# Kernel tuning notes

Measured on AMD Instinct MI355X. Metric: run time of the kernel, lower is better.

The kernel has to match this reference:

```python
import jax, jax.numpy as jnp
import numpy as np

DIM, HEADS, RANK = 768, 12, 64
HEAD_DIM = DIM // HEADS

def _xavier(key, shape):
    fan_in, fan_out = shape[1], shape[0]
    std = (2.0 / (fan_in + fan_out)) ** 0.5
    return std * jax.random.normal(key, shape, dtype=jnp.float32)

def setup_inputs() -> dict:
    key = jax.random.key(0)
    ks = jax.random.split(key, 12)
    B, N = 8, 1024
    x = jax.random.normal(ks[0], (B, N, DIM), dtype=jnp.float32)
    params = {}
    for i, nm in enumerate(['Q', 'K', 'V']):
        params[f'W_{nm}0'] = _xavier(ks[1 + 3 * i], (DIM, RANK))
        params[f'W_{nm}1'] = _xavier(ks[2 + 3 * i], (HEADS, RANK))
        params[f'W_{nm}2'] = _xavier(ks[3 + 3 * i], (HEAD_DIM, RANK))
    proj_w = _xavier(ks[10], (DIM, DIM))
    proj_b = jnp.zeros((DIM,), dtype=jnp.float32)
    return dict(x=x, W_Q0=params['W_Q0'], W_Q1=params['W_Q1'], W_Q2=params['W_Q2'],
                W_K0=params['W_K0'], W_K1=params['W_K1'], W_K2=params['W_K2'],
                W_V0=params['W_V0'], W_V1=params['W_V1'], W_V2=params['W_V2'],
                proj_w=proj_w, proj_b=proj_b)

def _cp_proj(xh, W2, W1, W0, B, N, H, hd):
    # xh: [B,N,H,hd]; contract head_dim with W2 and heads with W1 -> [B,N,R], then expand to dim via W0
    t = jnp.einsum('blnd,dr,nr->blr', xh, W2, W1)
    out = jnp.einsum('blr,mr->blm', t, W0)          # [B,N,dim]
    return out.reshape(B, N, H, hd).transpose(0, 2, 1, 3)  # [B,H,N,hd]

def reference(x, W_Q0, W_Q1, W_Q2, W_K0, W_K1, W_K2, W_V0, W_V1, W_V2, proj_w, proj_b):
    B, N, C = x.shape
    H = W_Q1.shape[0]
    hd = C // H
    scale = hd ** -0.5
    xh = x.reshape(B, N, H, hd)
    q = _cp_proj(xh, W_Q2, W_Q1, W_Q0, B, N, H, hd)
    k = _cp_proj(xh, W_K2, W_K1, W_K0, B, N, H, hd)
    v = _cp_proj(xh, W_V2, W_V1, W_V0, B, N, H, hd)
    attn = jax.nn.softmax(jnp.einsum('bhqd,bhkd->bhqk', q, k) * scale, axis=-1)
    out = jnp.einsum('bhqk,bhkd->bhqd', attn, v).transpose(0, 2, 1, 3).reshape(B, N, C)
    return out @ proj_w.T + proj_b
```

## Files before the change

### kernel.cpp

```cpp
#include <hip/hip_runtime.h>

typedef unsigned short u16;
typedef __attribute__((ext_vector_type(8))) short bf16x8;
typedef __attribute__((ext_vector_type(4))) float f32x4;
typedef __attribute__((ext_vector_type(4))) unsigned short u16x4;
typedef __attribute__((ext_vector_type(8))) unsigned short u16x8;

#define AS1 __attribute__((address_space(1)))
#define AS3 __attribute__((address_space(3)))

__device__ __forceinline__ float b2f(u16 s) {
    return __uint_as_float(((unsigned)s) << 16);
}
__device__ __forceinline__ u16 f2b(float f) {
    unsigned u = __float_as_uint(f);
    unsigned r = 0x7fffu + ((u >> 16) & 1u);
    return (u16)((u + r) >> 16);
}

__device__ __forceinline__ unsigned packtrunc(float p0, float p1) {
#if __has_builtin(__builtin_amdgcn_perm)
    return __builtin_amdgcn_perm(__float_as_uint(p1), __float_as_uint(p0), 0x07060302u);
#else
    return (__float_as_uint(p0) >> 16) | (__float_as_uint(p1) & 0xffff0000u);
#endif
}

__device__ __forceinline__ float truncbf(float p) {
    return __uint_as_float(__float_as_uint(p) & 0xffff0000u);
}

__device__ __forceinline__ void g2l16(const u16* g, u16* l) {
    __builtin_amdgcn_global_load_lds((const AS1 void*)g, (AS3 void*)l, 16, 0, 0);
}

#if __has_builtin(__builtin_amdgcn_exp2f)
#define EXP2(x) __builtin_amdgcn_exp2f(x)
#else
#define EXP2(x) exp2f(x)
#endif

__global__ __launch_bounds__(256) void build_prep(
    const float* __restrict__ Wq0, const float* __restrict__ Wq1, const float* __restrict__ Wq2,
    const float* __restrict__ Wk0, const float* __restrict__ Wk1, const float* __restrict__ Wk2,
    const float* __restrict__ Wv0, const float* __restrict__ Wv1, const float* __restrict__ Wv2,
    const float* __restrict__ PW,
    u16* __restrict__ G, u16* __restrict__ MqkT, u16* __restrict__ Dcat)
{
    const int bx = blockIdx.x;
    const int t = threadIdx.x;
    if (bx < 576) {
        const int idx = bx * 256 + t;
        const int row = idx / 768, c = idx - row * 768;
        const int which = row >> 6, r = row & 63;
        const int h = c >> 6, d = c & 63;
        const float* W1 = (which == 0) ? Wq1 : (which == 1) ? Wk1 : Wv1;
        const float* W2 = (which == 0) ? Wq2 : (which == 1) ? Wk2 : Wv2;
        G[idx] = f2b(W1[h * 64 + r] * W2[d * 64 + r]);
    } else if (bx < 624) {
        __shared__ float wq[64 * 65];
        __shared__ float wk[64 * 65];
        const int hq = bx - 576;
        const int h = hq >> 2, quarter = hq & 3;
        const float qs = 0.125f * 1.4426950408889634f;
        for (int i = t; i < 4096; i += 256) {
            const int dd = i >> 6, r = i & 63;
            wq[dd * 65 + r] = Wq0[(h * 64 + dd) * 64 + r] * qs;
            wk[dd * 65 + r] = Wk0[(h * 64 + dd) * 64 + r];
        }
        __syncthreads();
        const int j0 = quarter * 1024 + t * 4;
        const int r2 = j0 >> 6, r1b = j0 & 63;
        u16x4 pk;
#pragma unroll
        for (int jj = 0; jj < 4; ++jj) {
            float acc = 0.f;
#pragma unroll
            for (int dd = 0; dd < 64; ++dd)
                acc += wk[dd * 65 + r2] * wq[dd * 65 + r1b + jj];
            ((u16*)&pk)[jj] = f2b(acc);
        }
        *(u16x4*)(MqkT + (size_t)(h * 64 + r2) * 64 + r1b) = pk;
    } else {
        __shared__ float w0s[64 * 65];
        __shared__ float pws[32 * 65];
        const int hb = bx - 624;
        const int h = hb / 24, mBase = (hb - h * 24) * 32;
        for (int i = t; i < 4096; i += 256) {
            const int d = i >> 6, r = i & 63;
            w0s[d * 65 + r] = Wv0[(h * 64 + d) * 64 + r];
        }
        for (int i = t; i < 2048; i += 256) {
            const int mi = i >> 6, d = i & 63;
            pws[mi * 65 + d] = PW[(size_t)(mBase + mi) * 768 + h * 64 + d];
        }
        __syncthreads();
        const int r = t & 63, mi0 = t >> 6;
        float w0c[64];
#pragma unroll
        for (int d = 0; d < 64; ++d) w0c[d] = w0s[d * 65 + r];
        for (int mi = mi0; mi < 32; mi += 4) {
            float acc = 0.f;
#pragma unroll
            for (int d = 0; d < 64; ++d) acc += pws[mi * 65 + d] * w0c[d];
            Dcat[(size_t)(mBase + mi) * 768 + h * 64 + r] = f2b(acc);
        }
    }
}

__global__ __launch_bounds__(256, 2) void gemm_t(
    const float* __restrict__ X, const u16* __restrict__ G,
    u16* __restrict__ T, u16* __restrict__ tvt)
{
    __shared__ u16 As[64 * 32];
    __shared__ u16 Bs[64 * 32];

    const int tid = threadIdx.x;
    const int lane = tid & 63, wv = tid >> 6;
    const int l15 = lane & 15, quad = lane >> 4;

    const int lin = blockIdx.x + 3 * blockIdx.y;
    const int xcd = lin & 7, j = lin >> 3;
    const int col = j % 3, rowhi = j / 3;
    const int rowBase = (rowhi * 8 + xcd) * 64;
    const int colBase = col * 64;

    const int srow = tid >> 2;
    const int scol = (tid & 3) * 8;
    const float* aS = X + (size_t)(rowBase + srow) * 768 + scol;
    const u16*  bS  = G + (size_t)(colBase + srow) * 768 + scol;

    float4 a0 = *(const float4*)(aS);
    float4 a1 = *(const float4*)(aS + 4);
    int4   b0 = *(const int4*)(bS);

    const f32x4 zero4 = {0.f, 0.f, 0.f, 0.f};
    f32x4 acc[4];
#pragma unroll
    for (int tn = 0; tn < 4; ++tn) acc[tn] = zero4;

    for (int kk = 0; kk < 768; kk += 32) {
        __syncthreads();
        u16x8 ap;
        ap[0] = f2b(a0.x); ap[1] = f2b(a0.y); ap[2] = f2b(a0.z); ap[3] = f2b(a0.w);
        ap[4] = f2b(a1.x); ap[5] = f2b(a1.y); ap[6] = f2b(a1.z); ap[7] = f2b(a1.w);
        *(u16x8*)&As[srow * 32 + scol] = ap;
        *(int4*)&Bs[srow * 32 + scol]  = b0;
        __syncthreads();

        if (kk < 736) {
            a0 = *(const float4*)(aS + kk + 32);
            a1 = *(const float4*)(aS + kk + 36);
            b0 = *(const int4*)(bS + kk + 32);
        }

        const bf16x8 af = *(const bf16x8*)(As + (wv * 16 + l15) * 32 + quad * 8);
#pragma unroll
        for (int tn = 0; tn < 4; ++tn) {
            const bf16x8 bf = *(const bf16x8*)(Bs + (tn * 16 + l15) * 32 + quad * 8);
            acc[tn] = __builtin_amdgcn_mfma_f32_16x16x32_bf16(af, bf, acc[tn], 0, 0, 0);
        }
    }

    if (colBase < 128) {
#pragma unroll
        for (int tn = 0; tn < 4; ++tn) {
            const int c = colBase + tn * 16 + l15;
#pragma unroll
            for (int r = 0; r < 4; ++r) {
                const int grow = rowBase + wv * 16 + quad * 4 + r;
                T[(size_t)grow * 128 + c] = f2b(acc[tn][r]);
            }
        }
    } else {
#pragma unroll
        for (int tn = 0; tn < 4; ++tn) {
            const int rr = tn * 16 + l15;
            const int grow = rowBase + wv * 16 + quad * 4;
            u16x4 pk;
            pk.x = f2b(acc[tn][0]); pk.y = f2b(acc[tn][1]);
            pk.z = f2b(acc[tn][2]); pk.w = f2b(acc[tn][3]);
            *(u16x4*)(tvt + (size_t)rr * 8192 + grow) = pk;
        }
    }
}

__global__ __launch_bounds__(256, 3) void flash_attn9(
    const u16* __restrict__ T, const u16* __restrict__ MqkT,
    const u16* __restrict__ tvt, u16* __restrict__ Z)
{
    const int bh = blockIdx.x;
    const int qt = blockIdx.y;
    const int b = bh / 12, h = bh - b * 12;
    const u16* qp = T + ((size_t)b * 1024 + qt * 128) * 128;
    const u16* kp = T + (size_t)b * 1024 * 128 + 64;
    const u16* vp = tvt + b * 1024;

    __shared__ u16 B0raw[2 * 64 * 72];
    __shared__ u16 B1raw[2 * 64 * 72];

    const int t = threadIdx.x;
    const int lane = t & 63, wv = t >> 6;
    const int l15 = lane & 15, quad = lane >> 4;

    bf16x8 qf[2][2];
#pragma unroll
    for (int qg = 0; qg < 2; ++qg) {
        const u16* qrow = qp + (size_t)(wv * 32 + qg * 16 + l15) * 128;
        qf[qg][0] = *(const bf16x8*)(qrow + quad * 8);
        qf[qg][1] = *(const bf16x8*)(qrow + 32 + quad * 8);
    }

    const int srow = t >> 2;
    const int scol = (t & 3) * 16;
    const int p5 = srow & 31;
    const int lrow = (srow & 32) | ((p5 & 4) << 2) | ((p5 & 16) >> 1)
                   | ((p5 & 8) >> 1) | (p5 & 3);

    int4 kr0 = *(const int4*)(kp + (size_t)srow * 128 + scol);
    int4 kr1 = *(const int4*)(kp + (size_t)srow * 128 + scol + 8);
    int4 vr0 = *(const int4*)(vp + (size_t)srow * 8192 + scol);
    int4 vr1 = *(const int4*)(vp + (size_t)srow * 8192 + scol + 8);

    const f32x4 zero4 = {0.f, 0.f, 0.f, 0.f};
    {
        f32x4 Wt[2][4];
#pragma unroll
        for (int qg = 0; qg < 2; ++qg)
#pragma unroll
            for (int tn = 0; tn < 4; ++tn) Wt[qg][tn] = zero4;
#pragma unroll
        for (int ks = 0; ks < 2; ++ks) {
#pragma unroll
            for (int tn = 0; tn < 4; ++tn) {
                const bf16x8 mb = *(const bf16x8*)(
                    MqkT + (size_t)(h * 64 + tn * 16 + l15) * 64 + ks * 32 + quad * 8);
                Wt[0][tn] = __builtin_amdgcn_mfma_f32_16x16x32_bf16(qf[0][ks], mb, Wt[0][tn], 0, 0, 0);
                Wt[1][tn] = __builtin_amdgcn_mfma_f32_16x16x32_bf16(qf[1][ks], mb, Wt[1][tn], 0, 0, 0);
            }
        }
#pragma unroll
        for (int qg = 0; qg < 2; ++qg)
#pragma unroll
            for (int tn = 0; tn < 4; ++tn)
#pragma unroll
                for (int r = 0; r < 4; ++r)
                    B1raw[(wv * 32 + qg * 16 + quad * 4 + r) * 72 + tn * 16 + l15] =
                        f2b(Wt[qg][tn][r]);
    }
    __syncthreads();
    bf16x8 wf[2][2];
#pragma unroll
    for (int qg = 0; qg < 2; ++qg) {
        wf[qg][0] = *(const bf16x8*)&B1raw[(wv * 32 + qg * 16 + l15) * 72 + quad * 8];
        wf[qg][1] = *(const bf16x8*)&B1raw[(wv * 32 + qg * 16 + l15) * 72 + 32 + quad * 8];
    }

    *(int4*)&B0raw[lrow * 72 + scol]                 = kr0;
    *(int4*)&B0raw[lrow * 72 + scol + 8]             = kr1;
    *(int4*)&B0raw[64 * 72 + srow * 72 + scol]       = vr0;
    *(int4*)&B0raw[64 * 72 + srow * 72 + scol + 8]   = vr1;
    kr0 = *(const int4*)(kp + (size_t)(64 + srow) * 128 + scol);
    kr1 = *(const int4*)(kp + (size_t)(64 + srow) * 128 + scol + 8);
    vr0 = *(const int4*)(vp + (size_t)srow * 8192 + 64 + scol);
    vr1 = *(const int4*)(vp + (size_t)srow * 8192 + 64 + scol + 8);
    __syncthreads();

    f32x4 o_acc[2][4];
    float Lsum[2] = {0.f, 0.f};
#pragma unroll
    for (int qg = 0; qg < 2; ++qg)
#pragma unroll
        for (int tn = 0; tn < 4; ++tn) o_acc[qg][tn] = zero4;

    for (int kt = 0; kt < 16; ++kt) {
        u16* const kb = (kt & 1) ? B1raw : B0raw;
        u16* const vb = kb + 64 * 72;
        if (kt < 15) {
            u16* const kn = (kt & 1) ? B0raw : B1raw;
            *(int4*)&kn[lrow * 72 + scol]               = kr0;
            *(int4*)&kn[lrow * 72 + scol + 8]           = kr1;
            *(int4*)&kn[64 * 72 + srow * 72 + scol]     = vr0;
            *(int4*)&kn[64 * 72 + srow * 72 + scol + 8] = vr1;
            if (kt < 14) {
                kr0 = *(const int4*)(kp + (size_t)((kt + 2) * 64 + srow) * 128 + scol);
                kr1 = *(const int4*)(kp + (size_t)((kt + 2) * 64 + srow) * 128 + scol + 8);
                vr0 = *(const int4*)(vp + (size_t)srow * 8192 + (kt + 2) * 64 + scol);
                vr1 = *(const int4*)(vp + (size_t)srow * 8192 + (kt + 2) * 64 + scol + 8);
            }
        }

        f32x4 Sacc[2][4];
#pragma unroll
        for (int qg = 0; qg < 2; ++qg)
#pragma unroll
            for (int tk = 0; tk < 4; ++tk) Sacc[qg][tk] = zero4;
        __builtin_amdgcn_s_setprio(1);
#pragma unroll
        for (int ks = 0; ks < 2; ++ks) {
#pragma unroll
            for (int tk = 0; tk < 4; ++tk) {
                const bf16x8 kf = *(const bf16x8*)&kb[(tk * 16 + l15) * 72 + ks * 32 + quad * 8];
                Sacc[0][tk] = __builtin_amdgcn_mfma_f32_16x16x32_bf16(kf, wf[0][ks], Sacc[0][tk], 0, 0, 0);
                Sacc[1][tk] = __builtin_amdgcn_mfma_f32_16x16x32_bf16(kf, wf[1][ks], Sacc[1][tk], 0, 0, 0);
            }
        }
        __builtin_amdgcn_s_setprio(0);

        union { bf16x8 v; unsigned u[4]; } pf[2][2];
#pragma unroll
        for (int qg = 0; qg < 2; ++qg)
#pragma unroll
            for (int tk = 0; tk < 4; ++tk) {
                const float p0 = EXP2(Sacc[qg][tk][0]);
                const float p1 = EXP2(Sacc[qg][tk][1]);
                const float p2 = EXP2(Sacc[qg][tk][2]);
                const float p3 = EXP2(Sacc[qg][tk][3]);
                const int g = tk >> 1, hf = (tk & 1) * 2;
                pf[qg][g].u[hf + 0] = packtrunc(p0, p1);
                pf[qg][g].u[hf + 1] = packtrunc(p2, p3);
                Lsum[qg] += (truncbf(p0) + truncbf(p1)) + (truncbf(p2) + truncbf(p3));
            }

        __builtin_amdgcn_s_setprio(1);
#pragma unroll
        for (int g = 0; g < 2; ++g) {
#pragma unroll
            for (int tn = 0; tn < 4; ++tn) {
                const bf16x8 vf = *(const bf16x8*)&vb[(tn * 16 + l15) * 72 + g * 32 + quad * 8];
                o_acc[0][tn] = __builtin_amdgcn_mfma_f32_16x16x32_bf16(pf[0][g].v, vf, o_acc[0][tn], 0, 0, 0);
                o_acc[1][tn] = __builtin_amdgcn_mfma_f32_16x16x32_bf16(pf[1][g].v, vf, o_acc[1][tn], 0, 0, 0);
            }
        }
        __builtin_amdgcn_s_setprio(0);

        __syncthreads();
    }

#pragma unroll
    for (int qg = 0; qg < 2; ++qg) {
        float Ls = Lsum[qg];
        Ls += __shfl_xor(Ls, 16, 64);
        Ls += __shfl_xor(Ls, 32, 64);
#pragma unroll
        for (int r = 0; r < 4; ++r) {
            const float Lv = __shfl(Ls, quad * 4 + r, 64);
            const float inv = 1.0f / Lv;
            const int token = qt * 128 + wv * 32 + qg * 16 + quad * 4 + r;
#pragma unroll
            for (int tn = 0; tn < 4; ++tn) {
                const int col = h * 64 + tn * 16 + l15;
                Z[(size_t)(b * 1024 + token) * 768 + col] = f2b(o_acc[qg][tn][r] * inv);
            }
        }
    }
}

__global__ __launch_bounds__(256, 3) void gemm_out(
    const u16* __restrict__ A, const u16* __restrict__ Bt,
    float* __restrict__ C, const float* __restrict__ bias)
{
    __shared__ u16 As[128 * 32];
    __shared__ u16 Bs[64 * 32];

    const int tid  = threadIdx.x;
    const int lane = tid & 63, wv = tid >> 6;
    const int l15  = lane & 15, quad = lane >> 4;

    const int lin = blockIdx.x + 12 * blockIdx.y;
    const int xcd = lin & 7, j = lin >> 3;
    const int colT = j % 12, rowhi = j / 12;
    const int rowBase = (rowhi * 8 + xcd) * 128;
    const int colBase = colT * 64;

    const int srowA = wv * 32 + (lane >> 2);
    const int srowB = wv * 16 + (lane >> 2);
    const int scol  = (lane & 3) * 8;
    const u16* aSrc = A  + (size_t)(rowBase + srowA) * 768 + scol;
    const u16* bSrc = Bt + (size_t)(colBase + srowB) * 768 + scol;
    u16* aDst = As + wv * 1024;
    u16* bDst = Bs + wv * 512;

    const f32x4 zero4 = {0.f, 0.f, 0.f, 0.f};
    f32x4 acc[2][4];
#pragma unroll
    for (int tm = 0; tm < 2; ++tm)
#pragma unroll
        for (int tn = 0; tn < 4; ++tn) acc[tm][tn] = zero4;

    for (int kk = 0; kk < 768; kk += 32) {
        __syncthreads();
        g2l16(aSrc + kk,            aDst);
        g2l16(aSrc + kk + 16 * 768, aDst + 512);
        g2l16(bSrc + kk,            bDst);
        __syncthreads();

        bf16x8 af[2], bfm[4];
#pragma unroll
        for (int t = 0; t < 2; ++t)
            af[t]  = *(const bf16x8*)(As + (wv * 32 + t * 16 + l15) * 32 + quad * 8);
#pragma unroll
        for (int t = 0; t < 4; ++t)
            bfm[t] = *(const bf16x8*)(Bs + (t * 16 + l15) * 32 + quad * 8);
#pragma unroll
        for (int tm = 0; tm < 2; ++tm)
#pragma unroll
            for (int tn = 0; tn < 4; ++tn)
                acc[tm][tn] = __builtin_amdgcn_mfma_f32_16x16x32_bf16(
                    af[tm], bfm[tn], acc[tm][tn], 0, 0, 0);
    }

#pragma unroll
    for (int tm = 0; tm < 2; ++tm) {
        const int grow = rowBase + wv * 32 + tm * 16 + quad * 4;
#pragma unroll
        for (int tn = 0; tn < 4; ++tn) {
            const int gcol = colBase + tn * 16 + l15;
            const float bv = bias[gcol];
#pragma unroll
            for (int r = 0; r < 4; ++r)
                C[(size_t)(grow + r) * 768 + gcol] = acc[tm][tn][r] + bv;
        }
    }
}

extern "C" void kernel_launch(void* const* d_in, const int* in_sizes, int n_in,
                              void* d_out, int out_size, void* d_ws, size_t ws_size,
                              hipStream_t stream)
{
    const float* x      = (const float*)d_in[0];
    const float* Wq0    = (const float*)d_in[1];
    const float* Wq1    = (const float*)d_in[2];
    const float* Wq2    = (const float*)d_in[3];
    const float* Wk0    = (const float*)d_in[4];
    const float* Wk1    = (const float*)d_in[5];
    const float* Wk2    = (const float*)d_in[6];
    const float* Wv0    = (const float*)d_in[7];
    const float* Wv1    = (const float*)d_in[8];
    const float* Wv2    = (const float*)d_in[9];
    const float* proj_w = (const float*)d_in[10];
    const float* proj_b = (const float*)d_in[11];
    float* outp = (float*)d_out;

    char* ws = (char*)d_ws;
    u16* T    = (u16*)ws;
    u16* tvt  = (u16*)(ws + 2097152);
    u16* G    = (u16*)(ws + 3145728);
    u16* MqkT = (u16*)(ws + 3440640);
    u16* Dcat = (u16*)(ws + 3538944);
    u16* Zcat = (u16*)(ws + 4718592);

    build_prep<<<912, 256, 0, stream>>>(Wq0, Wq1, Wq2, Wk0, Wk1, Wk2, Wv0, Wv1, Wv2,
                                        proj_w, G, MqkT, Dcat);
    gemm_t<<<dim3(3, 128), 256, 0, stream>>>(x, G, T, tvt);
    flash_attn9<<<dim3(96, 8), 256, 0, stream>>>(T, MqkT, tvt, Zcat);
    gemm_out<<<dim3(12, 64), 256, 0, stream>>>(Zcat, Dcat, outp, proj_b);
}
```

Baseline: 178.0 us.

## Compute softmax row sums via MFMA with ones vector and unroll K-loop by two

```diff
diff --git a/kernel.cpp b/kernel.cpp
--- a/kernel.cpp
+++ b/kernel.cpp
@@ -24,10 +24,6 @@
 #else
     return (__float_as_uint(p0) >> 16) | (__float_as_uint(p1) & 0xffff0000u);
 #endif
-}
-
-__device__ __forceinline__ float truncbf(float p) {
-    return __uint_as_float(__float_as_uint(p) & 0xffff0000u);
 }
 
 __device__ __forceinline__ void g2l16(const u16* g, u16* l) {
@@ -185,7 +181,7 @@
     }
 }
 
-__global__ __launch_bounds__(256, 3) void flash_attn9(
+__global__ __launch_bounds__(256, 3) void flash_attn10(
     const u16* __restrict__ T, const u16* __restrict__ MqkT,
     const u16* __restrict__ tvt, u16* __restrict__ Z)
 {
@@ -217,6 +213,12 @@
     const int lrow = (srow & 32) | ((p5 & 4) << 2) | ((p5 & 16) >> 1)
                    | ((p5 & 8) >> 1) | (p5 & 3);
 
+    bf16x8 vone = {};
+    if (l15 == 0) {
+#pragma unroll
+        for (int j = 0; j < 8; ++j) vone[j] = (short)0x3F80;
+    }
+
     int4 kr0 = *(const int4*)(kp + (size_t)srow * 128 + scol);
     int4 kr1 = *(const int4*)(kp + (size_t)srow * 128 + scol + 8);
     int4 vr0 = *(const int4*)(vp + (size_t)srow * 8192 + scol);
@@ -267,84 +269,91 @@
     __syncthreads();
 
     f32x4 o_acc[2][4];
-    float Lsum[2] = {0.f, 0.f};
+    f32x4 Lacc[2] = {zero4, zero4};
 #pragma unroll
     for (int qg = 0; qg < 2; ++qg)
 #pragma unroll
         for (int tn = 0; tn < 4; ++tn) o_acc[qg][tn] = zero4;
 
-    for (int kt = 0; kt < 16; ++kt) {
-        u16* const kb = (kt & 1) ? B1raw : B0raw;
-        u16* const vb = kb + 64 * 72;
-        if (kt < 15) {
-            u16* const kn = (kt & 1) ? B0raw : B1raw;
-            *(int4*)&kn[lrow * 72 + scol]               = kr0;
-            *(int4*)&kn[lrow * 72 + scol + 8]           = kr1;
-            *(int4*)&kn[64 * 72 + srow * 72 + scol]     = vr0;
-            *(int4*)&kn[64 * 72 + srow * 72 + scol + 8] = vr1;
-            if (kt < 14) {
-                kr0 = *(const int4*)(kp + (size_t)((kt + 2) * 64 + srow) * 128 + scol);
-                kr1 = *(const int4*)(kp + (size_t)((kt + 2) * 64 + srow) * 128 + scol + 8);
-                vr0 = *(const int4*)(vp + (size_t)srow * 8192 + (kt + 2) * 64 + scol);
-                vr1 = *(const int4*)(vp + (size_t)srow * 8192 + (kt + 2) * 64 + scol + 8);
-            }
-        }
-
-        f32x4 Sacc[2][4];
-#pragma unroll
-        for (int qg = 0; qg < 2; ++qg)
-#pragma unroll
-            for (int tk = 0; tk < 4; ++tk) Sacc[qg][tk] = zero4;
-        __builtin_amdgcn_s_setprio(1);
-#pragma unroll
-        for (int ks = 0; ks < 2; ++ks) {
-#pragma unroll
-            for (int tk = 0; tk < 4; ++tk) {
-                const bf16x8 kf = *(const bf16x8*)&kb[(tk * 16 + l15) * 72 + ks * 32 + quad * 8];
-                Sacc[0][tk] = __builtin_amdgcn_mfma_f32_16x16x32_bf16(kf, wf[0][ks], Sacc[0][tk], 0, 0, 0);
-                Sacc[1][tk] = __builtin_amdgcn_mfma_f32_16x16x32_bf16(kf, wf[1][ks], Sacc[1][tk], 0, 0, 0);
-            }
-        }
-        __builtin_amdgcn_s_setprio(0);
-
-        union { bf16x8 v; unsigned u[4]; } pf[2][2];
-#pragma unroll
-        for (int qg = 0; qg < 2; ++qg)
-#pragma unroll
-            for (int tk = 0; tk < 4; ++tk) {
-                const float p0 = EXP2(Sacc[qg][tk][0]);
-                const float p1 = EXP2(Sacc[qg][tk][1]);
-                const float p2 = EXP2(Sacc[qg][tk][2]);
-                const float p3 = EXP2(Sacc[qg][tk][3]);
-                const int g = tk >> 1, hf = (tk & 1) * 2;
-                pf[qg][g].u[hf + 0] = packtrunc(p0, p1);
-                pf[qg][g].u[hf + 1] = packtrunc(p2, p3);
-                Lsum[qg] += (truncbf(p0) + truncbf(p1)) + (truncbf(p2) + truncbf(p3));
-            }
-
-        __builtin_amdgcn_s_setprio(1);
-#pragma unroll
-        for (int g = 0; g < 2; ++g) {
-#pragma unroll
-            for (int tn = 0; tn < 4; ++tn) {
-                const bf16x8 vf = *(const bf16x8*)&vb[(tn * 16 + l15) * 72 + g * 32 + quad * 8];
-                o_acc[0][tn] = __builtin_amdgcn_mfma_f32_16x16x32_bf16(pf[0][g].v, vf, o_acc[0][tn], 0, 0, 0);
-                o_acc[1][tn] = __builtin_amdgcn_mfma_f32_16x16x32_bf16(pf[1][g].v, vf, o_acc[1][tn], 0, 0, 0);
-            }
-        }
-        __builtin_amdgcn_s_setprio(0);
-
-        __syncthreads();
-    }
+#define STAGE(NB)                                                               \
+    {                                                                           \
+        *(int4*)&NB[lrow * 72 + scol]               = kr0;                      \
+        *(int4*)&NB[lrow * 72 + scol + 8]           = kr1;                      \
+        *(int4*)&NB[64 * 72 + srow * 72 + scol]     = vr0;                      \
+        *(int4*)&NB[64 * 72 + srow * 72 + scol + 8] = vr1;                      \
+    }
+#define PREFETCH(KT)                                                            \
+    {                                                                           \
+        kr0 = *(const int4*)(kp + (size_t)((KT) * 64 + srow) * 128 + scol);     \
+        kr1 = *(const int4*)(kp + (size_t)((KT) * 64 + srow) * 128 + scol + 8); \
+        vr0 = *(const int4*)(vp + (size_t)srow * 8192 + (KT) * 64 + scol);      \
+        vr1 = *(const int4*)(vp + (size_t)srow * 8192 + (KT) * 64 + scol + 8);  \
+    }
+#define FLASH_TILE(KB)                                                          \
+    {                                                                           \
+        f32x4 Sacc[2][4];                                                       \
+        _Pragma("unroll")                                                       \
+        for (int qg = 0; qg < 2; ++qg)                                          \
+            _Pragma("unroll")                                                   \
+            for (int tk = 0; tk < 4; ++tk) Sacc[qg][tk] = zero4;                \
+        _Pragma("unroll")                                                       \
+        for (int ks = 0; ks < 2; ++ks) {                                        \
+            _Pragma("unroll")                                                   \
+            for (int tk = 0; tk < 4; ++tk) {                                    \
+                const bf16x8 kf = *(const bf16x8*)&KB[(tk * 16 + l15) * 72 + ks * 32 + quad * 8]; \
+                Sacc[0][tk] = __builtin_amdgcn_mfma_f32_16x16x32_bf16(kf, wf[0][ks], Sacc[0][tk], 0, 0, 0); \
+                Sacc[1][tk] = __builtin_amdgcn_mfma_f32_16x16x32_bf16(kf, wf[1][ks], Sacc[1][tk], 0, 0, 0); \
+            }                                                                   \
+        }                                                                       \
+        union { bf16x8 v; unsigned u[4]; } pf[2][2];                            \
+        _Pragma("unroll")                                                       \
+        for (int qg = 0; qg < 2; ++qg)                                          \
+            _Pragma("unroll")                                                   \
+            for (int tk = 0; tk < 4; ++tk) {                                    \
+                const float p0 = EXP2(Sacc[qg][tk][0]);                         \
+                const float p1 = EXP2(Sacc[qg][tk][1]);                         \
+                const float p2 = EXP2(Sacc[qg][tk][2]);                         \
+                const float p3 = EXP2(Sacc[qg][tk][3]);                         \
+                const int g = tk >> 1, hf = (tk & 1) * 2;                       \
+                pf[qg][g].u[hf + 0] = packtrunc(p0, p1);                        \
+                pf[qg][g].u[hf + 1] = packtrunc(p2, p3);                        \
+            }                                                                   \
+        _Pragma("unroll")                                                       \
+        for (int g = 0; g < 2; ++g) {                                           \
+            _Pragma("unroll")                                                   \
+            for (int tn = 0; tn < 4; ++tn) {                                    \
+                const bf16x8 vf = *(const bf16x8*)&KB[64 * 72 + (tn * 16 + l15) * 72 + g * 32 + quad * 8]; \
+                o_acc[0][tn] = __builtin_amdgcn_mfma_f32_16x16x32_bf16(pf[0][g].v, vf, o_acc[0][tn], 0, 0, 0); \
+                o_acc[1][tn] = __builtin_amdgcn_mfma_f32_16x16x32_bf16(pf[1][g].v, vf, o_acc[1][tn], 0, 0, 0); \
+            }                                                                   \
+            Lacc[0] = __builtin_amdgcn_mfma_f32_16x16x32_bf16(pf[0][g].v, vone, Lacc[0], 0, 0, 0); \
+            Lacc[1] = __builtin_amdgcn_mfma_f32_16x16x32_bf16(pf[1][g].v, vone, Lacc[1], 0, 0, 0); \
+        }                                                                       \
+    }
+
+    for (int t8 = 0; t8 < 8; ++t8) {
+        const int kt0 = 2 * t8;
+        STAGE(B1raw);
+        if (t8 < 7) PREFETCH(kt0 + 2);
+        FLASH_TILE(B0raw);
+        __syncthreads();
+        if (t8 < 7) {
+            STAGE(B0raw);
+            PREFETCH(kt0 + 3);
+        }
+        FLASH_TILE(B1raw);
+        if (t8 < 7) __syncthreads();
+    }
+
+#undef STAGE
+#undef PREFETCH
+#undef FLASH_TILE
 
 #pragma unroll
     for (int qg = 0; qg < 2; ++qg) {
-        float Ls = Lsum[qg];
-        Ls += __shfl_xor(Ls, 16, 64);
-        Ls += __shfl_xor(Ls, 32, 64);
 #pragma unroll
         for (int r = 0; r < 4; ++r) {
-            const float Lv = __shfl(Ls, quad * 4 + r, 64);
+            const float Lv = __shfl(Lacc[qg][r], quad << 4, 64);
             const float inv = 1.0f / Lv;
             const int token = qt * 128 + wv * 32 + qg * 16 + quad * 4 + r;
 #pragma unroll
@@ -453,6 +462,6 @@
     build_prep<<<912, 256, 0, stream>>>(Wq0, Wq1, Wq2, Wk0, Wk1, Wk2, Wv0, Wv1, Wv2,
                                         proj_w, G, MqkT, Dcat);
     gemm_t<<<dim3(3, 128), 256, 0, stream>>>(x, G, T, tvt);
-    flash_attn9<<<dim3(96, 8), 256, 0, stream>>>(T, MqkT, tvt, Zcat);
+    flash_attn10<<<dim3(96, 8), 256, 0, stream>>>(T, MqkT, tvt, Zcat);
     gemm_out<<<dim3(12, 64), 256, 0, stream>>>(Zcat, Dcat, outp, proj_b);
 }
```

After: 172.2 us. 1.03x faster.
